# Optimization experiments

Hardware: AMD Instinct MI355X
Metric: run time of the kernel (lower is better)

## Reference

```python
import jax, jax.numpy as jnp
import numpy as np

H = 8   # num_key_value_heads
G = 4   # num_query_heads // num_key_value_heads
HQ = H * G  # 32 query heads


def setup_inputs() -> dict:
    key = jax.random.key(0)
    k0, k1, k2, k3 = jax.random.split(key, 4)
    B, N, D = 2, 2048, 2048
    s = 1.0 / np.sqrt(D)
    x = jax.random.normal(k0, (B, N, D), jnp.float32)
    Wq = jax.random.normal(k1, (D, D), jnp.float32) * s
    Wkv = jax.random.normal(k2, (D, 2 * D // G), jnp.float32) * s
    Wp = jax.random.normal(k3, (D, D), jnp.float32) * s
    bp = jnp.zeros((D,), jnp.float32)
    return {"x": x, "Wq": Wq, "Wkv": Wkv, "Wp": Wp, "bp": bp}


def reference(x, Wq, Wkv, Wp, bp):
    B, N, D = x.shape
    C = D // (H * G)  # head dim
    scale = float(np.sqrt(HQ))  # module scales by sqrt(num_query_heads)
    q = (x @ Wq) / scale                     # [B, N, D]
    kv = x @ Wkv                             # [B, N, 2*H*C]
    k, v = jnp.split(kv, 2, axis=-1)         # each [B, N, H*C]
    # q: b n (h g c) -> b g h n c
    q = q.reshape(B, N, H, G, C).transpose(0, 3, 2, 1, 4)
    # k, v: b s (h c) -> b h s c
    k = k.reshape(B, N, H, C).transpose(0, 2, 1, 3)
    v = v.reshape(B, N, H, C).transpose(0, 2, 1, 3)
    sim = jnp.einsum('bghnc,bhsc->bghns', q, k)
    attn = jax.nn.softmax(sim, axis=-1)
    o = jnp.einsum('bghns,bhsc->bghnc', attn, v)
    # b g h n c -> b n (h g c)
    o = o.transpose(0, 3, 2, 1, 4).reshape(B, N, D)
    return o @ Wp + bp
```

## Files before the change

### kernel.cpp

```cpp
#include <hip/hip_runtime.h>
#include <math.h>

typedef __attribute__((ext_vector_type(8))) __bf16 bf16x8;
typedef __attribute__((ext_vector_type(4))) float f32x4;
typedef __attribute__((ext_vector_type(16))) float f32x16;
typedef __attribute__((ext_vector_type(2))) unsigned u32x2;

#define MFMA16(a, b, c) __builtin_amdgcn_mfma_f32_16x16x32_bf16((a), (b), (c), 0, 0, 0)
#define MFMA32(a, b, c) __builtin_amdgcn_mfma_f32_32x32x16_bf16((a), (b), (c), 0, 0, 0)

#define GLOAD_LDS(g, l)                                                                     \
  __builtin_amdgcn_global_load_lds((const __attribute__((address_space(1))) unsigned int*)(g), \
                                   (__attribute__((address_space(3))) unsigned int*)(l), 16, 0, 0)

static constexpr int Bb  = 2;
static constexpr int Nn  = 2048;
static constexpr int Dd  = 2048;
static constexpr int Hh  = 8;
static constexpr int Gg  = 4;
static constexpr int Cc  = 64;
static constexpr int KVW = 1024;

__device__ __forceinline__ unsigned short f2bf(float f) {
  unsigned int u = __float_as_uint(f);
  u += 0x7FFFu + ((u >> 16) & 1u);
  return (unsigned short)(u >> 16);
}

__device__ __forceinline__ float xhalf_sum(float v) {
  u32x2 r = __builtin_amdgcn_permlane32_swap(__float_as_uint(v), __float_as_uint(v), false, false);
  return __uint_as_float(r.x) + __uint_as_float(r.y);
}

__global__ void xconv(const float* __restrict__ x, unsigned short* __restrict__ xb, int n4) {
  int i = blockIdx.x * blockDim.x + threadIdx.x;
  const int stride = gridDim.x * blockDim.x;
  for (; i < n4; i += stride) {
    float4 v = ((const float4*)x)[i];
    ushort4 o;
    o.x = f2bf(v.x); o.y = f2bf(v.y); o.z = f2bf(v.z); o.w = f2bf(v.w);
    ((ushort4*)xb)[i] = o;
  }
}

__global__ void wconv(const float* __restrict__ W, unsigned short* __restrict__ Wt,
                      int K, int N, float scale) {
  __shared__ float t[32][33];
  const int n0 = blockIdx.x * 32, k0 = blockIdx.y * 32;
  for (int i = threadIdx.x; i < 1024; i += blockDim.x) {
    int r = i >> 5, c = i & 31;
    t[r][c] = W[(size_t)(k0 + r) * N + n0 + c];
  }
  __syncthreads();
  for (int i = threadIdx.x; i < 1024; i += blockDim.x) {
    int r = i >> 5, c = i & 31;
    Wt[(size_t)(n0 + r) * K + k0 + c] = f2bf(t[c][r] * scale);
  }
}

__global__ void vtrans(const unsigned short* __restrict__ kvb, unsigned short* __restrict__ vT) {
  __shared__ unsigned short t[64][72];
  const int s0 = blockIdx.x * 64;
  const int b = blockIdx.y >> 3, h = blockIdx.y & 7;
  const unsigned short* src = kvb + ((size_t)b * Nn + s0) * KVW + Hh * Cc + h * Cc;
  for (int i = threadIdx.x; i < 4096; i += blockDim.x) {
    int s = i >> 6, c = i & 63;
    t[s][c] = src[(size_t)s * KVW + c];
  }
  __syncthreads();
  unsigned short* dst = vT + (size_t)(b * Hh + h) * Cc * Nn + s0;
  for (int i = threadIdx.x; i < 4096; i += blockDim.x) {
    int c = i >> 6, s = i & 63;
    dst[(size_t)c * Nn + s] = t[s][c];
  }
}

template <bool OUTF32>
__global__ __launch_bounds__(256, 2)
void gemm_bt(const unsigned short* __restrict__ A, const unsigned short* __restrict__ Bt,
             unsigned short* __restrict__ Cb, float* __restrict__ Cf,
             const float* __restrict__ bias, int M, int N, int K) {
  __shared__ unsigned short As[128 * 40];
  __shared__ unsigned short Bs[128 * 40];
  const int tid = threadIdx.x;
  const size_t m0 = (size_t)blockIdx.x * 128;
  const size_t n0 = (size_t)blockIdx.y * 128;
  const int nk = K >> 5;

  const int c0 = tid, c1 = tid + 256;
  const int r0 = c0 >> 2, kp0 = (c0 & 3) << 3;
  const int r1 = c1 >> 2, kp1 = (c1 & 3) << 3;
  const unsigned short* Ap0 = A + (m0 + r0) * (size_t)K + kp0;
  const unsigned short* Ap1 = A + (m0 + r1) * (size_t)K + kp1;
  const unsigned short* Bp0 = Bt + (n0 + r0) * (size_t)K + kp0;
  const unsigned short* Bp1 = Bt + (n0 + r1) * (size_t)K + kp1;
  const int sa0 = r0 * 40 + kp0, sa1 = r1 * 40 + kp1;

  bf16x8 va0 = *(const bf16x8*)Ap0;
  bf16x8 va1 = *(const bf16x8*)Ap1;
  bf16x8 vb0 = *(const bf16x8*)Bp0;
  bf16x8 vb1 = *(const bf16x8*)Bp1;

  const int wid = tid >> 6, lane = tid & 63;
  const int wr = wid >> 1, wc = wid & 1;
  const int lrow = lane & 15, lg = lane >> 4, lk = lg << 3;
  const int abase = (wr * 64 + lrow) * 40 + lk;
  const int bbase = (wc * 64 + lrow) * 40 + lk;

  const f32x4 zero = {0.f, 0.f, 0.f, 0.f};
  f32x4 acc[4][4];
#pragma unroll
  for (int i = 0; i < 4; ++i)
#pragma unroll
    for (int j = 0; j < 4; ++j) acc[i][j] = zero;

  for (int kt = 0; kt < nk; ++kt) {
    __syncthreads();
    *(bf16x8*)&As[sa0] = va0;
    *(bf16x8*)&As[sa1] = va1;
    *(bf16x8*)&Bs[sa0] = vb0;
    *(bf16x8*)&Bs[sa1] = vb1;
    __syncthreads();
    if (kt + 1 < nk) {
      const size_t ko = (size_t)(kt + 1) << 5;
      va0 = *(const bf16x8*)(Ap0 + ko);
      va1 = *(const bf16x8*)(Ap1 + ko);
      vb0 = *(const bf16x8*)(Bp0 + ko);
      vb1 = *(const bf16x8*)(Bp1 + ko);
    }
    bf16x8 af[4], bfr[4];
#pragma unroll
    for (int mt = 0; mt < 4; ++mt) af[mt] = *(const bf16x8*)&As[abase + mt * 16 * 40];
#pragma unroll
    for (int nt = 0; nt < 4; ++nt) bfr[nt] = *(const bf16x8*)&Bs[bbase + nt * 16 * 40];
#pragma unroll
    for (int mt = 0; mt < 4; ++mt)
#pragma unroll
      for (int nt = 0; nt < 4; ++nt) acc[mt][nt] = MFMA16(af[mt], bfr[nt], acc[mt][nt]);
  }

#pragma unroll
  for (int mt = 0; mt < 4; ++mt)
#pragma unroll
    for (int nt = 0; nt < 4; ++nt) {
      const size_t col = n0 + wc * 64 + nt * 16 + lrow;
#pragma unroll
      for (int i = 0; i < 4; ++i) {
        const size_t r = m0 + wr * 64 + mt * 16 + lg * 4 + i;
        if constexpr (OUTF32)
          Cf[r * N + col] = acc[mt][nt][i] + bias[col];
        else
          Cb[r * N + col] = f2bf(acc[mt][nt][i]);
      }
    }
}

__global__ __launch_bounds__(512, 4)
void attn_kernel(const unsigned short* __restrict__ qb, const unsigned short* __restrict__ kvb,
                 const unsigned short* __restrict__ vT, unsigned short* __restrict__ ob) {
  __shared__ unsigned short Ks[2][4096];
  __shared__ unsigned short Vs[2][4096];
  const int tid = threadIdx.x;
  const int wid = tid >> 6, lane = tid & 63;
  const int r31 = lane & 31, hi = lane >> 5, r7 = r31 & 7;
  const int q0 = blockIdx.x * 256 + wid * 32;
  const int bhg = blockIdx.y;
  const int b = bhg >> 5, h = (bhg >> 2) & 7, g = bhg & 3;

  const unsigned short* kptr = kvb + (size_t)b * Nn * KVW + h * Cc;
  const unsigned short* vptr = vT + (size_t)(b * Hh + h) * Cc * Nn;

  const int sub = lane >> 3, slot = lane & 7;
  const int gslot = slot ^ sub;
  const unsigned short* gk = kptr + (size_t)(wid * 8 + sub) * KVW + gslot * 8;
  const unsigned short* gv = vptr + (size_t)(wid * 8 + sub) * Nn + gslot * 8;

  bf16x8 qf[4];
  {
    const unsigned short* qrow =
        qb + ((size_t)b * Nn + q0 + r31) * Dd + h * (Gg * Cc) + g * Cc + hi * 8;
#pragma unroll
    for (int ks = 0; ks < 4; ++ks) qf[ks] = *(const bf16x8*)(qrow + ks * 16);
  }

  int off[4];
#pragma unroll
  for (int ks = 0; ks < 4; ++ks) off[ks] = r31 * 128 + (((2 * ks + hi) ^ r7) << 4);

  f32x16 O0 = (f32x16)0.0f, O1 = (f32x16)0.0f;
  float L_ = 0.0f;

  auto stage = [&](int bi) {
    GLOAD_LDS(gk, &Ks[bi][wid * 512]);
    GLOAD_LDS(gv, &Vs[bi][wid * 512]);
    gk += (size_t)64 * KVW;
    gv += 64;
  };

  auto compute = [&](const unsigned short* Kb_, const unsigned short* Vb_) {
    const char* Kb = (const char*)Kb_;
    const char* Vb = (const char*)Vb_;
    f32x16 S0 = (f32x16)0.0f, S1 = (f32x16)0.0f;
    __builtin_amdgcn_s_setprio(1);
#pragma unroll
    for (int ks = 0; ks < 4; ++ks) {
      bf16x8 k0 = *(const bf16x8*)(Kb + off[ks]);
      bf16x8 k1 = *(const bf16x8*)(Kb + off[ks] + 4096);
      S0 = MFMA32(k0, qf[ks], S0);
      S1 = MFMA32(k1, qf[ks], S1);
    }
    __builtin_amdgcn_s_setprio(0);
    float rs = 0.0f;
    unsigned pk[16];
#pragma unroll
    for (int kt2 = 0; kt2 < 2; ++kt2)
#pragma unroll
      for (int blk = 0; blk < 4; ++blk)
#pragma unroll
        for (int m = 0; m < 2; ++m) {
          float pa = exp2f(kt2 ? S1[4 * blk + 2 * m] : S0[4 * blk + 2 * m]);
          float pb = exp2f(kt2 ? S1[4 * blk + 2 * m + 1] : S0[4 * blk + 2 * m + 1]);
          rs += pa + pb;
          asm("v_cvt_pk_bf16_f32 %0, %1, %2" : "=v"(pk[kt2 * 8 + blk * 2 + m]) : "v"(pa), "v"(pb));
        }
    L_ += xhalf_sum(rs);
    __builtin_amdgcn_s_setprio(1);
#pragma unroll
    for (int vs = 0; vs < 4; ++vs) {
      const int base = (vs >> 1) * 8 + (vs & 1) * 4;
      u32x2 rA = __builtin_amdgcn_permlane32_swap(pk[base + 0], pk[base + 2], false, false);
      u32x2 rB = __builtin_amdgcn_permlane32_swap(pk[base + 1], pk[base + 3], false, false);
      union { unsigned u[4]; bf16x8 v; } pf;
      pf.u[0] = rA.x; pf.u[1] = rB.x; pf.u[2] = rA.y; pf.u[3] = rB.y;
      bf16x8 v0 = *(const bf16x8*)(Vb + off[vs]);
      bf16x8 v1 = *(const bf16x8*)(Vb + off[vs] + 4096);
      O0 = MFMA32(pf.v, v0, O0);
      O1 = MFMA32(pf.v, v1, O1);
    }
    __builtin_amdgcn_s_setprio(0);
  };

  stage(0);
  __syncthreads();
  for (int t = 0; t < Nn / 64; t += 2) {
    stage(1);
    compute(Ks[0], Vs[0]);
    __syncthreads();
    if (t + 2 < Nn / 64) stage(0);
    compute(Ks[1], Vs[1]);
    __syncthreads();
  }

  float Linv = 1.0f / L_;
  const size_t orow_base = (size_t)b * Nn + q0;
  const int ocol = h * (Gg * Cc) + g * Cc;
#pragma unroll
  for (int r = 0; r < 16; ++r) {
    const int q_r = (r & 3) + 8 * (r >> 2) + 4 * hi;
    float li = __shfl(Linv, q_r);
    const size_t basep = (orow_base + q_r) * Dd + ocol;
    ob[basep + r31] = f2bf(O0[r] * li);
    ob[basep + 32 + r31] = f2bf(O1[r] * li);
  }
}

extern "C" void kernel_launch(void* const* d_in, const int* in_sizes, int n_in,
                              void* d_out, int out_size, void* d_ws, size_t ws_size,
                              hipStream_t stream) {
  const float* x   = (const float*)d_in[0];
  const float* Wq  = (const float*)d_in[1];
  const float* Wkv = (const float*)d_in[2];
  const float* Wp  = (const float*)d_in[3];
  const float* bp  = (const float*)d_in[4];
  float* out = (float*)d_out;

  char* ws = (char*)d_ws;
  size_t off = 0;
  auto alloc = [&](size_t bytes) {
    char* p = ws + off;
    off += (bytes + 255) & ~(size_t)255;
    return p;
  };
  unsigned short* xb   = (unsigned short*)alloc((size_t)Bb * Nn * Dd * 2);
  unsigned short* Wqt  = (unsigned short*)alloc((size_t)Dd * Dd * 2);
  unsigned short* Wkvt = (unsigned short*)alloc((size_t)KVW * Dd * 2);
  unsigned short* Wpt  = (unsigned short*)alloc((size_t)Dd * Dd * 2);
  unsigned short* qbf  = (unsigned short*)alloc((size_t)Bb * Nn * Dd * 2);
  unsigned short* kvb  = (unsigned short*)alloc((size_t)Bb * Nn * KVW * 2);
  unsigned short* vT   = (unsigned short*)alloc((size_t)Bb * Hh * Cc * Nn * 2);
  unsigned short* ob   = xb;

  const int M = Bb * Nn;
  const float qscale = 0.17677669529663687f * 1.4426950408889634f;

  xconv<<<2048, 256, 0, stream>>>(x, xb, (Bb * Nn * Dd) / 4);
  wconv<<<dim3(Dd / 32, Dd / 32), 256, 0, stream>>>(Wq, Wqt, Dd, Dd, qscale);
  wconv<<<dim3(KVW / 32, Dd / 32), 256, 0, stream>>>(Wkv, Wkvt, Dd, KVW, 1.0f);
  wconv<<<dim3(Dd / 32, Dd / 32), 256, 0, stream>>>(Wp, Wpt, Dd, Dd, 1.0f);

  gemm_bt<false><<<dim3(M / 128, Dd / 128), 256, 0, stream>>>(xb, Wqt, qbf, nullptr, nullptr, M, Dd, Dd);
  gemm_bt<false><<<dim3(M / 128, KVW / 128), 256, 0, stream>>>(xb, Wkvt, kvb, nullptr, nullptr, M, KVW, Dd);
  vtrans<<<dim3(Nn / 64, Bb * Hh), 256, 0, stream>>>(kvb, vT);
  attn_kernel<<<dim3(Nn / 256, Bb * Hh * Gg), 512, 0, stream>>>(qbf, kvb, vT, ob);
  gemm_bt<true><<<dim3(M / 128, Dd / 128), 256, 0, stream>>>(ob, Wpt, nullptr, out, bp, M, Dd, Dd);
}
```

Before: 259.0 us.

## Double-buffer GEMM tiles with direct global-to-LDS loads and XOR swizzle

Rewrites the GEMM main loop so tiles are copied straight from global memory into LDS with global_load_lds, instead of going through registers. The K tile grows from 32 to 64, the LDS buffers are doubled, and the load of the next tile overlaps MFMA work on the current one. An XOR swizzle on the 16-byte slots replaces the padded layout to avoid bank conflicts. The cost is more LDS per block (64KB), which may hurt occupancy under launch_bounds(256,2), and correctness depends on nk being even and on async-load ordering at the barriers.

```diff
diff --git a/kernel.cpp b/kernel.cpp
--- a/kernel.cpp
+++ b/kernel.cpp
@@ -80,32 +80,49 @@
 void gemm_bt(const unsigned short* __restrict__ A, const unsigned short* __restrict__ Bt,
              unsigned short* __restrict__ Cb, float* __restrict__ Cf,
              const float* __restrict__ bias, int M, int N, int K) {
-  __shared__ unsigned short As[128 * 40];
-  __shared__ unsigned short Bs[128 * 40];
+  __shared__ unsigned short As[2][128 * 64];
+  __shared__ unsigned short Bs[2][128 * 64];
   const int tid = threadIdx.x;
+  const int wid = tid >> 6, lane = tid & 63;
   const size_t m0 = (size_t)blockIdx.x * 128;
   const size_t n0 = (size_t)blockIdx.y * 128;
-  const int nk = K >> 5;
-
-  const int c0 = tid, c1 = tid + 256;
-  const int r0 = c0 >> 2, kp0 = (c0 & 3) << 3;
-  const int r1 = c1 >> 2, kp1 = (c1 & 3) << 3;
-  const unsigned short* Ap0 = A + (m0 + r0) * (size_t)K + kp0;
-  const unsigned short* Ap1 = A + (m0 + r1) * (size_t)K + kp1;
-  const unsigned short* Bp0 = Bt + (n0 + r0) * (size_t)K + kp0;
-  const unsigned short* Bp1 = Bt + (n0 + r1) * (size_t)K + kp1;
-  const int sa0 = r0 * 40 + kp0, sa1 = r1 * 40 + kp1;
-
-  bf16x8 va0 = *(const bf16x8*)Ap0;
-  bf16x8 va1 = *(const bf16x8*)Ap1;
-  bf16x8 vb0 = *(const bf16x8*)Bp0;
-  bf16x8 vb1 = *(const bf16x8*)Bp1;
-
-  const int wid = tid >> 6, lane = tid & 63;
+  const int nk = K >> 6;
+
+  const int sub = lane >> 3, slot = lane & 7;
+  const int gslot = slot ^ sub;
+  const unsigned short* gA[4];
+  const unsigned short* gB[4];
+#pragma unroll
+  for (int i = 0; i < 4; ++i) {
+    const int c = wid * 4 + i;
+    gA[i] = A + (m0 + c * 8 + sub) * (size_t)K + gslot * 8;
+    gB[i] = Bt + (n0 + c * 8 + sub) * (size_t)K + gslot * 8;
+  }
+
+  auto stage = [&](int bi) {
+#pragma unroll
+    for (int i = 0; i < 4; ++i) {
+      const int c = wid * 4 + i;
+      GLOAD_LDS(gA[i], &As[bi][c * 512]);
+      GLOAD_LDS(gB[i], &Bs[bi][c * 512]);
+      gA[i] += 64;
+      gB[i] += 64;
+    }
+  };
+
   const int wr = wid >> 1, wc = wid & 1;
-  const int lrow = lane & 15, lg = lane >> 4, lk = lg << 3;
-  const int abase = (wr * 64 + lrow) * 40 + lk;
-  const int bbase = (wc * 64 + lrow) * 40 + lk;
+  const int lrow = lane & 15, lg = lane >> 4;
+  int aoff[4][2], boff[4][2];
+#pragma unroll
+  for (int mt = 0; mt < 4; ++mt)
+#pragma unroll
+    for (int kc = 0; kc < 2; ++kc) {
+      const int ra = wr * 64 + mt * 16 + lrow;
+      const int rb = wc * 64 + mt * 16 + lrow;
+      const int sl = (((kc << 2) + lg) ^ (lrow & 7)) << 4;
+      aoff[mt][kc] = ra * 128 + sl;
+      boff[mt][kc] = rb * 128 + sl;
+    }
 
   const f32x4 zero = {0.f, 0.f, 0.f, 0.f};
   f32x4 acc[4][4];
@@ -114,29 +131,32 @@
 #pragma unroll
     for (int j = 0; j < 4; ++j) acc[i][j] = zero;
 
-  for (int kt = 0; kt < nk; ++kt) {
+  auto compute = [&](int bi) {
+    const char* Ab = (const char*)&As[bi][0];
+    const char* Bb2 = (const char*)&Bs[bi][0];
+#pragma unroll
+    for (int kc = 0; kc < 2; ++kc) {
+      bf16x8 af[4], bfr[4];
+#pragma unroll
+      for (int mt = 0; mt < 4; ++mt) af[mt] = *(const bf16x8*)(Ab + aoff[mt][kc]);
+#pragma unroll
+      for (int nt = 0; nt < 4; ++nt) bfr[nt] = *(const bf16x8*)(Bb2 + boff[nt][kc]);
+#pragma unroll
+      for (int mt = 0; mt < 4; ++mt)
+#pragma unroll
+        for (int nt = 0; nt < 4; ++nt) acc[mt][nt] = MFMA16(af[mt], bfr[nt], acc[mt][nt]);
+    }
+  };
+
+  stage(0);
+  __syncthreads();
+  for (int kt = 0; kt < nk; kt += 2) {
+    stage(1);
+    compute(0);
     __syncthreads();
-    *(bf16x8*)&As[sa0] = va0;
-    *(bf16x8*)&As[sa1] = va1;
-    *(bf16x8*)&Bs[sa0] = vb0;
-    *(bf16x8*)&Bs[sa1] = vb1;
+    if (kt + 2 < nk) stage(0);
+    compute(1);
     __syncthreads();
-    if (kt + 1 < nk) {
-      const size_t ko = (size_t)(kt + 1) << 5;
-      va0 = *(const bf16x8*)(Ap0 + ko);
-      va1 = *(const bf16x8*)(Ap1 + ko);
-      vb0 = *(const bf16x8*)(Bp0 + ko);
-      vb1 = *(const bf16x8*)(Bp1 + ko);
-    }
-    bf16x8 af[4], bfr[4];
-#pragma unroll
-    for (int mt = 0; mt < 4; ++mt) af[mt] = *(const bf16x8*)&As[abase + mt * 16 * 40];
-#pragma unroll
-    for (int nt = 0; nt < 4; ++nt) bfr[nt] = *(const bf16x8*)&Bs[bbase + nt * 16 * 40];
-#pragma unroll
-    for (int mt = 0; mt < 4; ++mt)
-#pragma unroll
-      for (int nt = 0; nt < 4; ++nt) acc[mt][nt] = MFMA16(af[mt], bfr[nt], acc[mt][nt]);
   }
 
 #pragma unroll
```

Result: faster. 252.6 us (-2.5%).
